# Kernel optimization log

Hardware: AMD Instinct MI355X
Metric: run time of the kernel (lower is better)

## Reference

```python
import jax, jax.numpy as jnp
import numpy as np

B, S, T, D, H, V, R = 16, 100, 60, 512, 8, 32000, 20
DK = D // H
WIN = 20
DECAY1 = (jnp.arange(WIN, dtype=jnp.float32) + 1.0) / 20.0  # decay1[i] = (i+1)/20


def _add_state_init():
    # decay2[:S] padded with zeros: decay2[i] = 1 - (i+1)/50 for i < 50
    idx = jnp.arange(S, dtype=jnp.float32)
    return jnp.where(idx < 50, 1.0 - (idx + 1.0) / 50.0, 0.0)  # [S]


def _forward(v_outputs, f_outputs, query_seq, attn_logits, Wr, br, Wa, ba, Wq_lin,
             Wn, bn, Wlogit, blogit, Wptr, bptr, Wqr, bqr, Wkr, bkr, src_mask):
    dt = v_outputs.dtype
    add0 = _add_state_init().astype(dt)
    mem0 = v_outputs * add0[None, :, None]                       # [B,S,D]
    add_state0 = jnp.broadcast_to(add0[None, :, None], (B, S, 1)).astype(dt)
    # role_selector keys, computed once (queries change per step)
    k_heads = (f_outputs @ Wkr + bkr).reshape(B, R, H, DK).transpose(0, 2, 1, 3)  # [B,H,R,DK]
    abuf0 = jnp.zeros((WIN, B, S), dt)   # last-20 attn weights (oldest first)
    qbuf0 = jnp.zeros((WIN, B, D), dt)   # last-20 decoder states

    def step(carry, xs):
        mem, add_state, abuf, qbuf, t = carry
        logits_t, q_t = xs               # [B,S], [B,D]
        # masked softmax over frames (uniformed_this in original)
        attn_i = jax.nn.softmax(jnp.where(src_mask, logits_t, -jnp.inf), axis=-1)  # [B,S]
        # memory read: selected_frame = bmm(attn, memory_bank)
        sel = jnp.einsum('bs,bsd->bd', attn_i, mem)
        # role_selector multi-head attention weights (mean over heads)
        qh = (sel @ Wqr + bqr).reshape(B, H, DK)
        scores = jnp.einsum('bhk,bhrk->bhr', qh, k_heads) / jnp.sqrt(jnp.asarray(DK, dt))
        role_attn = jax.nn.softmax(scores, axis=-1).mean(axis=1)  # [B,R]
        # pointer-generator joint distribution
        vocab = q_t @ Wlogit.T + blogit                            # [B,V] (tied embedding)
        p_gen = jax.nn.sigmoid(q_t @ Wptr + bptr)                  # [B,1]
        joint = jnp.concatenate([vocab, role_attn * p_gen], axis=-1)  # [B,V+R]
        # slide 20-step window buffers
        abuf = jnp.concatenate([abuf[1:], attn_i[None]], axis=0)
        qbuf = jnp.concatenate([qbuf[1:], q_t[None]], axis=0)
        # decay-weighted sums: temp = softmax(decay1[20-L:]) over valid window
        L = jnp.minimum(t + 1, WIN)
        w = jax.nn.softmax(jnp.where(jnp.arange(WIN) >= WIN - L, DECAY1, -jnp.inf)).astype(dt)
        attn_w = jnp.einsum('k,kbs->bs', w, abuf)                  # [B,S]
        query_w = jnp.einsum('k,kbd->bd', w, qbuf)                 # [B,D]
        # gated remove
        rem = jax.nn.sigmoid(q_t @ Wr + br)[:, :, None]            # [B,1,1]
        addp = jax.nn.sigmoid(q_t @ Wa + ba)[:, :, None]           # [B,1,1]
        sim = jax.nn.sigmoid(jnp.einsum('bsd,bd->bs', mem, query_w @ Wq_lin.T))[:, :, None]
        mem = mem * (1.0 - rem * attn_w[:, :, None] * sim)
        # gated add
        last_ctx = jnp.einsum('bs,bsd->bd', attn_w, v_outputs)[:, None, :]  # [B,1,D]
        nxt = jax.nn.sigmoid(
            jnp.concatenate([v_outputs, jnp.broadcast_to(last_ctx, (B, S, D))], axis=-1) @ Wn + bn)  # [B,S,1]
        gain = addp * nxt
        mem = mem + v_outputs * (1.0 - add_state) * gain
        add_state = add_state + (1.0 - add_state) * gain
        return (mem, add_state, abuf, qbuf, t + 1), joint

    xs = (attn_logits.transpose(1, 0, 2), query_seq.transpose(1, 0, 2))
    _, joints = jax.lax.scan(step, (mem0, add_state0, abuf0, qbuf0, 0), xs)
    return joints.transpose(1, 0, 2)  # [B,T,V+R]


def setup_inputs() -> dict:
    key = jax.random.key(0)
    ks = jax.random.split(key, 12)
    n = jax.random.normal
    sd = 0.02
    return {
        'v_outputs': n(ks[0], (B, S, D), jnp.float32),
        'f_outputs': n(ks[1], (B, R, D), jnp.float32),
        'query_seq': n(ks[2], (B, T, D), jnp.float32),
        'attn_logits': n(ks[3], (B, T, S), jnp.float32),
        'Wr': n(ks[4], (D, 1), jnp.float32) * sd, 'br': jnp.zeros((1,), jnp.float32),
        'Wa': n(ks[5], (D, 1), jnp.float32) * sd, 'ba': jnp.zeros((1,), jnp.float32),
        'Wq_lin': n(ks[6], (D, D), jnp.float32) * sd,
        'Wn': n(ks[7], (2 * D, 1), jnp.float32) * sd, 'bn': jnp.zeros((1,), jnp.float32),
        'Wlogit': n(ks[8], (V, D), jnp.float32) * sd, 'blogit': jnp.zeros((V,), jnp.float32),
        'Wptr': n(ks[9], (D, 1), jnp.float32) * sd, 'bptr': jnp.zeros((1,), jnp.float32),
        'Wqr': n(ks[10], (D, D), jnp.float32) * sd, 'bqr': jnp.zeros((D,), jnp.float32),
        'Wkr': n(ks[11], (D, D), jnp.float32) * sd, 'bkr': jnp.zeros((D,), jnp.float32),
        'src_mask': jnp.ones((B, S), dtype=bool),
    }


def reference(v_outputs, f_outputs, query_seq, attn_logits, Wr, br, Wa, ba, Wq_lin,
              Wn, bn, Wlogit, blogit, Wptr, bptr, Wqr, bqr, Wkr, bkr, src_mask):
    return _forward(v_outputs, f_outputs, query_seq, attn_logits, Wr, br, Wa, ba, Wq_lin,
                    Wn, bn, Wlogit, blogit, Wptr, bptr, Wqr, bqr, Wkr, bkr, src_mask)
```

## Files before the change

kernel.cpp:

```cpp
#include <hip/hip_runtime.h>
#include <math.h>

constexpr int B = 16, S = 100, T = 60, D = 512, H = 8, V = 32000, R = 20;
constexpr int DK = 64, WIN = 20;
constexpr int VR = V + R;
constexpr int BT = B * T;
constexpr int MP = 1024;
constexpr int TP = 64;
constexpr int FP = 384;
constexpr int VBP = 1664;

typedef unsigned short u16;
typedef __attribute__((ext_vector_type(8))) short bf16x8;
typedef __attribute__((ext_vector_type(4))) float f32x4;

__device__ __forceinline__ float wred_sum(float v) {
#pragma unroll
  for (int st = 32; st > 0; st >>= 1) v += __shfl_xor(v, st, 64);
  return v;
}
__device__ __forceinline__ float wred_max(float v) {
#pragma unroll
  for (int st = 32; st > 0; st >>= 1) v = fmaxf(v, __shfl_xor(v, st, 64));
  return v;
}
__device__ __forceinline__ float sigmoidf_(float x) { return 1.f / (1.f + expf(-x)); }
__device__ __forceinline__ u16 f2bf(float x) {
  unsigned u = __float_as_uint(x);
  return (u16)((u + 0x7fffu + ((u >> 16) & 1u)) >> 16);
}
__device__ __forceinline__ void gload_lds16(const u16* g, u16* l) {
  __builtin_amdgcn_global_load_lds((const __attribute__((address_space(1))) void*)g,
                                   (__attribute__((address_space(3))) void*)l, 16, 0, 0);
}


__device__ __forceinline__ void vn_body(int row, int l, const float* __restrict__ v,
                                        const float* __restrict__ Wn,
                                        float* __restrict__ vn, float* __restrict__ vn2) {
  const float* vr = v + (size_t)row * D + l * 8;
  float p0 = 0.f, p1 = 0.f;
#pragma unroll
  for (int i = 0; i < 8; i++) {
    float x = vr[i];
    p0 = fmaf(x, Wn[l * 8 + i], p0);
    p1 = fmaf(x, Wn[D + l * 8 + i], p1);
  }
  p0 = wred_sum(p0); p1 = wred_sum(p1);
  if (l == 0) { vn[row] = p0; vn2[row] = p1; }
}

__device__ __forceinline__ void attnscal_body(int row, int l,
    const float* __restrict__ logits, const float* __restrict__ q,
    const float* __restrict__ Wr, const float* __restrict__ br,
    const float* __restrict__ Wa, const float* __restrict__ ba,
    const float* __restrict__ Wptr, const float* __restrict__ bptr,
    float* __restrict__ attn_g, float* __restrict__ remv,
    float* __restrict__ addp, float* __restrict__ pgen) {
  const float* src = logits + (size_t)row * S;
  float a = src[l];
  float b2 = (l + 64 < S) ? src[l + 64] : -INFINITY;
  float m = wred_max(fmaxf(a, b2));
  float ea = expf(a - m), eb = (l + 64 < S) ? expf(b2 - m) : 0.f;
  float inv = 1.f / wred_sum(ea + eb);
  attn_g[(size_t)row * S + l] = ea * inv;
  if (l + 64 < S) attn_g[(size_t)row * S + l + 64] = eb * inv;

  const float* qr = q + (size_t)row * D + l * 8;
  float pr = 0.f, pa = 0.f, pp = 0.f;
#pragma unroll
  for (int i = 0; i < 8; i++) {
    float x = qr[i];
    pr = fmaf(x, Wr[l * 8 + i], pr);
    pa = fmaf(x, Wa[l * 8 + i], pa);
    pp = fmaf(x, Wptr[l * 8 + i], pp);
  }
#pragma unroll
  for (int st = 32; st > 0; st >>= 1) {
    pr += __shfl_xor(pr, st, 64);
    pa += __shfl_xor(pa, st, 64);
    pp += __shfl_xor(pp, st, 64);
  }
  if (l == 0) {
    remv[row] = sigmoidf_(pr + br[0]);
    addp[row] = sigmoidf_(pa + ba[0]);
    pgen[row] = sigmoidf_(pp + bptr[0]);
  }
}

__device__ __forceinline__ void attnw_body(int row, int tid, float* red,
    const float* __restrict__ attn, const float* __restrict__ vn2,
    const float* __restrict__ remv, float* __restrict__ ra, float* __restrict__ ctxn) {
  int b = row / T, t = row % T;
  int L = min(t + 1, WIN);
  if (tid < 128) {
    float dnm = 0.f;
    for (int j = 0; j < L; j++) dnm += expf((float)(WIN - j) / 20.f);
    float p = 0.f;
    if (tid < S) {
      float aw = 0.f;
      for (int j = 0; j < L; j++)
        aw = fmaf(expf((float)(WIN - j) / 20.f) / dnm, attn[(size_t)(row - j) * S + tid], aw);
      ra[(size_t)row * S + tid] = remv[row] * aw;
      p = aw * vn2[b * S + tid];
    }
    red[tid] = p;
  }
  __syncthreads();
  if (tid < 64) {
    float v2 = red[tid] + red[tid + 64];
    v2 = wred_sum(v2);
    if (tid == 0) ctxn[row] = v2;
  }
}

constexpr int NW = V * D / 4;
constexpr int NQ = MP * D / 4;
constexpr int NWQ = D * D / 4;
constexpr int NF = FP * D / 4;
constexpr int NVB = VBP * D / 4;
constexpr int NB_CVT = (NW + NQ + NWQ + NF + NVB) / 256;
constexpr int NB_QWB = MP;
constexpr int NB_PREP = NB_CVT + NB_QWB + 128;
__device__ __forceinline__ void prep_body(int blk, int tid, float (*tile)[65],
    const float* __restrict__ Wlogit, const float* __restrict__ q,
    const float* __restrict__ Wq, const float* __restrict__ f, const float* __restrict__ v,
    const float* __restrict__ Wqr, const float* __restrict__ Wkr,
    u16* __restrict__ Wlbf, u16* __restrict__ qbf,
    u16* __restrict__ Wqlb, u16* __restrict__ fb, u16* __restrict__ vb,
    u16* __restrict__ qwb, u16* __restrict__ WqrT, u16* __restrict__ WkrT) {
  if (blk < NB_CVT) {
    int idx = blk * 256 + tid;
    if (idx < NW) {
      float4 x = reinterpret_cast<const float4*>(Wlogit)[idx];
      ushort4 o = {f2bf(x.x), f2bf(x.y), f2bf(x.z), f2bf(x.w)};
      reinterpret_cast<ushort4*>(Wlbf)[idx] = o;
    } else if (idx < NW + NQ) {
      int j = idx - NW;
      int row = (j * 4) / D;
      ushort4 o = {0, 0, 0, 0};
      if (row < BT) {
        float4 x = reinterpret_cast<const float4*>(q)[j];
        o = {f2bf(x.x), f2bf(x.y), f2bf(x.z), f2bf(x.w)};
      }
      reinterpret_cast<ushort4*>(qbf)[j] = o;
    } else if (idx < NW + NQ + NWQ) {
      int j = idx - NW - NQ;
      float4 x = reinterpret_cast<const float4*>(Wq)[j];
      ushort4 o = {f2bf(x.x), f2bf(x.y), f2bf(x.z), f2bf(x.w)};
      reinterpret_cast<ushort4*>(Wqlb)[j] = o;
    } else if (idx < NW + NQ + NWQ + NF) {
      int j = idx - NW - NQ - NWQ;
      int row = (j * 4) / D;
      ushort4 o = {0, 0, 0, 0};
      if (row < B * R) {
        float4 x = reinterpret_cast<const float4*>(f)[j];
        o = {f2bf(x.x), f2bf(x.y), f2bf(x.z), f2bf(x.w)};
      }
      reinterpret_cast<ushort4*>(fb)[j] = o;
    } else {
      int j = idx - NW - NQ - NWQ - NF;
      int row = (j * 4) / D;
      ushort4 o = {0, 0, 0, 0};
      if (row < B * S) {
        float4 x = reinterpret_cast<const float4*>(v)[j];
        o = {f2bf(x.x), f2bf(x.y), f2bf(x.z), f2bf(x.w)};
      }
      reinterpret_cast<ushort4*>(vb)[j] = o;
    }
  } else if (blk < NB_CVT + NB_QWB) {
    int row = blk - NB_CVT;
    if (row >= BT) {
      qwb[(size_t)row * D + tid] = 0; qwb[(size_t)row * D + tid + 256] = 0;
      return;
    }
    int t = row % T, L = min(t + 1, WIN);
    float dnm = 0.f;
    for (int j = 0; j < L; j++) dnm += expf((float)(WIN - j) / 20.f);
    float a0 = 0.f, a1 = 0.f;
    for (int j = 0; j < L; j++) {
      float wj = expf((float)(WIN - j) / 20.f) / dnm;
      a0 = fmaf(wj, q[(size_t)(row - j) * D + tid], a0);
      a1 = fmaf(wj, q[(size_t)(row - j) * D + tid + 256], a1);
    }
    qwb[(size_t)row * D + tid] = f2bf(a0);
    qwb[(size_t)row * D + tid + 256] = f2bf(a1);
  } else {
    int qt = blk - NB_CVT - NB_QWB;
    const float* src = (qt < 64) ? Wqr : Wkr;
    u16* dst = (qt < 64) ? WqrT : WkrT;
    int q64 = qt & 63;
    int bx = q64 % 8, by = q64 / 8;
#pragma unroll
    for (int i = 0; i < 16; i++) {
      int e = i * 256 + tid, r = e >> 6, c = e & 63;
      tile[r][c] = src[(size_t)(by * 64 + r) * D + bx * 64 + c];
    }
    __syncthreads();
#pragma unroll
    for (int i = 0; i < 16; i++) {
      int e = i * 256 + tid, r = e >> 6, c = e & 63;
      dst[(size_t)(bx * 64 + r) * D + by * 64 + c] = f2bf(tile[c][r]);
    }
  }
}

__device__ __forceinline__ void gemm512_body(const u16* __restrict__ A, const u16* __restrict__ Bw,
                                             const float* __restrict__ bias, float* __restrict__ outp,
                                             int mlimit, int mt, int nt, int tid, u16* ldsbuf) {
  u16* As = ldsbuf;
  u16* Bs = ldsbuf + 128 * 64;
  int m0 = mt * 128, n0 = nt * 128;
  int l = tid & 63;
  int w = tid >> 6, wm = w >> 1, wn = w & 1;
  f32x4 acc[4][4];
#pragma unroll
  for (int mb = 0; mb < 4; mb++)
#pragma unroll
    for (int nb = 0; nb < 4; nb++) acc[mb][nb] = (f32x4){0.f, 0.f, 0.f, 0.f};

  for (int k0 = 0; k0 < D; k0 += 64) {
#pragma unroll
    for (int i = 0; i < 4; i++) {
      int chunk = i * 256 + tid;
      int row = chunk >> 3, kc = chunk & 7;
      int kcs = kc ^ (row & 7);
      gload_lds16(A + (size_t)(m0 + row) * D + k0 + kcs * 8, As + chunk * 8);
      gload_lds16(Bw + (size_t)(n0 + row) * D + k0 + kcs * 8, Bs + chunk * 8);
    }
    __syncthreads();
#pragma unroll
    for (int kk = 0; kk < 2; kk++) {
      bf16x8 af[4], bfr[4];
#pragma unroll
      for (int mb = 0; mb < 4; mb++) {
        int row = wm * 64 + mb * 16 + (l & 15);
        int kc0 = kk * 4 + (l >> 4);
        af[mb] = *(const bf16x8*)(As + row * 64 + ((kc0 ^ (row & 7)) << 3));
      }
#pragma unroll
      for (int nb = 0; nb < 4; nb++) {
        int row = wn * 64 + nb * 16 + (l & 15);
        int kc0 = kk * 4 + (l >> 4);
        bfr[nb] = *(const bf16x8*)(Bs + row * 64 + ((kc0 ^ (row & 7)) << 3));
      }
#pragma unroll
      for (int mb = 0; mb < 4; mb++)
#pragma unroll
        for (int nb = 0; nb < 4; nb++)
          acc[mb][nb] = __builtin_amdgcn_mfma_f32_16x16x32_bf16(af[mb], bfr[nb], acc[mb][nb], 0, 0, 0);
    }
    __syncthreads();
  }

  float* ch = (float*)ldsbuf;
#pragma unroll
  for (int c = 0; c < 4; c++) {
    if (wm == (c >> 1)) {
#pragma unroll
      for (int nb = 0; nb < 4; nb++) {
        int col = wn * 64 + nb * 16 + (l & 15);
        float bl = bias ? bias[n0 + col] : 0.f;
#pragma unroll
        for (int mbi = 0; mbi < 2; mbi++) {
          int mb = (c & 1) * 2 + mbi;
#pragma unroll
          for (int q2 = 0; q2 < 4; q2++) {
            int row_local = mb * 16 + (l >> 4) * 4 + q2 - (c & 1) * 32;
            ch[row_local * 132 + col] = acc[mb][nb][q2] + bl;
          }
        }
      }
    }
    __syncthreads();
#pragma unroll
    for (int p = 0; p < 4; p++) {
      int r = p * 8 + (tid >> 5);
      int m = m0 + c * 32 + r;
      if (m < mlimit) {
        int seg = tid & 31;
        *(float4*)(outp + (size_t)m * D + n0 + seg * 4) =
            *(const float4*)(ch + r * 132 + seg * 4);
      }
    }
    __syncthreads();
  }
}

__device__ __forceinline__ void vocab_body(int bid, int tid, u16* ldsbuf,
    const u16* __restrict__ A, const u16* __restrict__ Bw,
    const float* __restrict__ blog, float* __restrict__ out) {
  u16* As = ldsbuf;
  u16* Bs = ldsbuf + 128 * 64;
  int swz = (bid & 7) * 250 + (bid >> 3);
  int m0 = (swz & 7) * 128, n0 = (swz >> 3) * 128;
  int l = tid & 63;
  int w = tid >> 6, wm = w >> 1, wn = w & 1;

  f32x4 acc[4][4];
#pragma unroll
  for (int mb = 0; mb < 4; mb++)
#pragma unroll
    for (int nb = 0; nb < 4; nb++) acc[mb][nb] = (f32x4){0.f, 0.f, 0.f, 0.f};

  for (int k0 = 0; k0 < D; k0 += 64) {
#pragma unroll
    for (int i = 0; i < 4; i++) {
      int chunk = i * 256 + tid;
      int row = chunk >> 3, kc = chunk & 7;
      int kcs = kc ^ (row & 7);
      gload_lds16(A + (size_t)(m0 + row) * D + k0 + kcs * 8, As + chunk * 8);
      gload_lds16(Bw + (size_t)(n0 + row) * D + k0 + kcs * 8, Bs + chunk * 8);
    }
    __syncthreads();
#pragma unroll
    for (int kk = 0; kk < 2; kk++) {
      bf16x8 af[4], bfr[4];
#pragma unroll
      for (int mb = 0; mb < 4; mb++) {
        int row = wm * 64 + mb * 16 + (l & 15);
        int kc0 = kk * 4 + (l >> 4);
        af[mb] = *(const bf16x8*)(As + row * 64 + ((kc0 ^ (row & 7)) << 3));
      }
#pragma unroll
      for (int nb = 0; nb < 4; nb++) {
        int row = wn * 64 + nb * 16 + (l & 15);
        int kc0 = kk * 4 + (l >> 4);
        bfr[nb] = *(const bf16x8*)(Bs + row * 64 + ((kc0 ^ (row & 7)) << 3));
      }
#pragma unroll
      for (int mb = 0; mb < 4; mb++)
#pragma unroll
        for (int nb = 0; nb < 4; nb++)
          acc[mb][nb] = __builtin_amdgcn_mfma_f32_16x16x32_bf16(af[mb], bfr[nb], acc[mb][nb], 0, 0, 0);
    }
    __syncthreads();
  }

  float* ch = (float*)ldsbuf;
#pragma unroll
  for (int c = 0; c < 4; c++) {
    if (wm == (c >> 1)) {
#pragma unroll
      for (int nb = 0; nb < 4; nb++) {
        int col = wn * 64 + nb * 16 + (l & 15);
        float bl = blog[n0 + col];
#pragma unroll
        for (int mbi = 0; mbi < 2; mbi++) {
          int mb = (c & 1) * 2 + mbi;
#pragma unroll
          for (int q2 = 0; q2 < 4; q2++) {
            int row_local = mb * 16 + (l >> 4) * 4 + q2 - (c & 1) * 32;
            ch[row_local * 132 + col] = acc[mb][nb][q2] + bl;
          }
        }
      }
    }
    __syncthreads();
#pragma unroll
    for (int p = 0; p < 4; p++) {
      int r = p * 8 + (tid >> 5);
      int m = m0 + c * 32 + r;
      if (m < BT) {
        int seg = tid & 31;
        *(float4*)(out + (size_t)m * VR + n0 + seg * 4) =
            *(const float4*)(ch + r * 132 + seg * 4);
      }
    }
    __syncthreads();
  }
}

__device__ __forceinline__ void qhgemm_body(int bq, int tid, float* gT ,
    const float* __restrict__ vWqr, const float* __restrict__ gammaT,
    const float* __restrict__ bqr, float* __restrict__ qh) {
  int b = bq >> 2, dc = bq & 3;
  int dl = tid & 127, th0 = tid >> 7;
  int d = dc * 128 + dl;
  for (int i = tid; i < S * TP; i += 256) {
    int r = i >> 6, c = i & 63;
    gT[r * TP + c] = gammaT[((size_t)b * S + r) * TP + c];
  }
  __syncthreads();
  float acc[2][16];
#pragma unroll
  for (int g = 0; g < 2; g++)
#pragma unroll
    for (int m = 0; m < 16; m++) acc[g][m] = 0.f;
  for (int ss = 0; ss < S; ss++) {
    float vv = vWqr[((size_t)b * S + ss) * D + d];
#pragma unroll
    for (int g = 0; g < 2; g++) {
      int tg = th0 + 2 * g;
      const float* gp = gT + ss * TP + tg * 16;
      float4 g0 = *(const float4*)gp;
      float4 g1 = *(const float4*)(gp + 4);
      float4 g2 = *(const float4*)(gp + 8);
      float4 g3 = *(const float4*)(gp + 12);
      acc[g][0]  = fmaf(g0.x, vv, acc[g][0]);  acc[g][1]  = fmaf(g0.y, vv, acc[g][1]);
      acc[g][2]  = fmaf(g0.z, vv, acc[g][2]);  acc[g][3]  = fmaf(g0.w, vv, acc[g][3]);
      acc[g][4]  = fmaf(g1.x, vv, acc[g][4]);  acc[g][5]  = fmaf(g1.y, vv, acc[g][5]);
      acc[g][6]  = fmaf(g1.z, vv, acc[g][6]);  acc[g][7]  = fmaf(g1.w, vv, acc[g][7]);
      acc[g][8]  = fmaf(g2.x, vv, acc[g][8]);  acc[g][9]  = fmaf(g2.y, vv, acc[g][9]);
      acc[g][10] = fmaf(g2.z, vv, acc[g][10]); acc[g][11] = fmaf(g2.w, vv, acc[g][11]);
      acc[g][12] = fmaf(g3.x, vv, acc[g][12]); acc[g][13] = fmaf(g3.y, vv, acc[g][13]);
      acc[g][14] = fmaf(g3.z, vv, acc[g][14]); acc[g][15] = fmaf(g3.w, vv, acc[g][15]);
    }
  }
  float bz = bqr[d];
#pragma unroll
  for (int g = 0; g < 2; g++) {
    int tg = th0 + 2 * g;
#pragma unroll
    for (int m = 0; m < 16; m++) {
      int t = tg * 16 + m;
      if (t < T) qh[((size_t)b * T + t) * D + d] = acc[g][m] + bz;
    }
  }
}

__device__ __forceinline__ void vubeta_body(int bq, int tid, float* sm,
    const float* __restrict__ u, const float* __restrict__ v,
    const float* __restrict__ attn, const float* __restrict__ ra,
    const float* __restrict__ addp, const float* __restrict__ ctxn,
    const float* __restrict__ vn, const float* __restrict__ bn,
    float* __restrict__ gammaT) {
  int b = bq / 5, sc = bq % 5;
  int tq = tid >> 2, sg = tid & 3;
  float* u_s = sm;
  float* v_s = sm + 7920;
  float* aw_s = sm + 10560;
  float* ra_s = sm + 11760;
  float* vu_s = sm + 12960;
  float* gm_s = sm + 14160;
  float* ap_s = sm + 15360;
  float* cx_s = sm + 15420;
  float* vns_s = sm + 15480;
#pragma unroll
  for (int ii = 0; ii < 5; ii++) {
    int i = ii * 256 + tid;
    if (i < T * 20) {
      int t = i / 20, sl = i % 20;
      size_t base = ((size_t)b * T + t) * S + sc * 20 + sl;
      aw_s[t * 20 + sl] = attn[base];
      ra_s[t * 20 + sl] = ra[base];
    }
  }
  if (tid < T) { ap_s[tid] = addp[b * T + tid]; cx_s[tid] = ctxn[b * T + tid]; }
  if (tid >= 64 && tid < 84) vns_s[tid - 64] = vn[b * S + sc * 20 + tid - 64];

  float acc[5] = {0, 0, 0, 0, 0};
  for (int kc = 0; kc < 4; kc++) {
#pragma unroll
    for (int ii = 0; ii < 8; ii++) {
      int i = ii * 256 + tid;
      if (i < 60 * 32) {
        int r = i >> 5, c = (i & 31) * 4;
        *(float4*)&u_s[r * 132 + c] =
            *(const float4*)&u[((size_t)b * T + r) * D + kc * 128 + c];
      }
    }
#pragma unroll
    for (int ii = 0; ii < 3; ii++) {
      int i = ii * 256 + tid;
      if (i < 20 * 32) {
        int r = i >> 5, c = (i & 31) * 4;
        *(float4*)&v_s[r * 132 + c] =
            *(const float4*)&v[((size_t)b * S + sc * 20 + r) * D + kc * 128 + c];
      }
    }
    __syncthreads();
    if (tq < 60) {
#pragma unroll
      for (int e0 = 0; e0 < 128; e0 += 4) {
        float4 uu = *(const float4*)&u_s[tq * 132 + e0];
#pragma unroll
        for (int m = 0; m < 5; m++) {
          float4 vv = *(const float4*)&v_s[(sg * 5 + m) * 132 + e0];
          acc[m] = fmaf(uu.x, vv.x, acc[m]);
          acc[m] = fmaf(uu.y, vv.y, acc[m]);
          acc[m] = fmaf(uu.z, vv.z, acc[m]);
          acc[m] = fmaf(uu.w, vv.w, acc[m]);
        }
      }
    }
    __syncthreads();
  }
  if (tq < 60) {
#pragma unroll
    for (int m = 0; m < 5; m++) vu_s[tq * 20 + sg * 5 + m] = acc[m];
  }
  __syncthreads();
  if (tid < 20) {
    int s = sc * 20 + tid;
    float dec = (s < 50) ? 1.f - (float)(s + 1) / 50.f : 0.f;
    float a = dec, beta = dec;
    float vns = vns_s[tid], bnv = bn[0];
    for (int t = 0; t < T; t++) {
      float g = ap_s[t] * sigmoidf_(vns + cx_s[t] + bnv);
      float wv = (1.f - a) * g;
      a += wv;
      gm_s[t * 20 + tid] = aw_s[t * 20 + tid] * beta;
      beta = beta * (1.f - ra_s[t * 20 + tid] * sigmoidf_(beta * vu_s[t * 20 + tid])) + wv;
    }
  }
  __syncthreads();
#pragma unroll
  for (int ii = 0; ii < 5; ii++) {
    int i = ii * 256 + tid;
    if (i < T * 20) {
      int sl = i / 60, t = i % 60;
      gammaT[((size_t)b * S + sc * 20 + sl) * TP + t] = gm_s[t * 20 + sl];
    }
  }
}

__device__ __forceinline__ void role_body(int row, int tid, float* sc, float* pr,
    const float* __restrict__ khf, const float* __restrict__ qh,
    const float* __restrict__ pgen, float* __restrict__ out) {
  int b = row / T;
  if (tid < H * R) {
    int h = tid / R, r = tid % R;
    const float* qp = qh + (size_t)row * D + h * DK;
    const float* kp = khf + (size_t)(b * R + r) * D + h * DK;
    float acc = 0.f;
#pragma unroll
    for (int i = 0; i < DK; i++) acc = fmaf(qp[i], kp[i], acc);
    sc[tid] = acc * 0.125f;
  }
  __syncthreads();
  if (tid < H) {
    float m = -INFINITY;
    for (int r = 0; r < R; r++) m = fmaxf(m, sc[tid * R + r]);
    float ssum = 0.f;
    for (int r = 0; r < R; r++) { float e = expf(sc[tid * R + r] - m); pr[tid * R + r] = e; ssum += e; }
    float inv = 1.f / ssum;
    for (int r = 0; r < R; r++) pr[tid * R + r] *= inv;
  }
  __syncthreads();
  if (tid < R) {
    float acc = 0.f;
#pragma unroll
    for (int h = 0; h < H; h++) acc += pr[h * R + tid];
    out[(size_t)row * VR + V + tid] = acc * (1.f / H) * pgen[row];
  }
}


__global__ __launch_bounds__(256) void k_combo1(
    const float* Wlogit, const float* q, const float* Wq, const float* f,
    const float* Wqr, const float* Wkr, const float* logits, const float* v,
    const float* Wn, const float* Wr, const float* br, const float* Wa, const float* ba,
    const float* Wptr, const float* bptr,
    u16* Wlbf, u16* qbf, u16* Wqlb, u16* fb, u16* vb, u16* qwb, u16* WqrT, u16* WkrT,
    float* vn, float* vn2, float* attn_g, float* remv, float* addp, float* pgen) {
  __shared__ float tile[64][65];
  int blk = blockIdx.x, tid = threadIdx.x;
  if (blk < NB_PREP) {
    prep_body(blk, tid, tile, Wlogit, q, Wq, f, v, Wqr, Wkr,
              Wlbf, qbf, Wqlb, fb, vb, qwb, WqrT, WkrT);
  } else if (blk < NB_PREP + 400) {
    int row = (blk - NB_PREP) * 4 + (tid >> 6);
    vn_body(row, tid & 63, v, Wn, vn, vn2);
  } else {
    int row = (blk - NB_PREP - 400) * 4 + (tid >> 6);
    attnscal_body(row, tid & 63, logits, q, Wr, br, Wa, ba, Wptr, bptr,
                  attn_g, remv, addp, pgen);
  }
}

__global__ __launch_bounds__(256) void k_combo2(
    const u16* qbf, const u16* Wlbf, const float* blog, float* out,
    const u16* qwb, const u16* Wqlb, float* u,
    const u16* fb, const u16* WkrT, const float* bkr, float* khf,
    const u16* vb, const u16* WqrT, float* vWqr,
    const float* attn, const float* vn2, const float* remv, float* ra, float* ctxn) {
  __shared__ u16 lds[2 * 128 * 64];
  int blk = blockIdx.x, tid = threadIdx.x;
  if (blk < 550) {
    vocab_body(blk, tid, lds, qbf, Wlbf, blog, out);
  } else if (blk < 594) {
    int z = blk - 550, xx = z % 11, yy = z / 11;
    if (xx < 8) gemm512_body(qwb, Wqlb, nullptr, u, BT, xx, yy, tid, lds);
    else        gemm512_body(fb, WkrT, bkr, khf, B * R, xx - 8, yy, tid, lds);
  } else if (blk < 646) {
    int z = blk - 594;
    gemm512_body(vb, WqrT, nullptr, vWqr, B * S, z % 13, z / 13, tid, lds);
  } else {
    attnw_body(blk - 646, tid, (float*)lds, attn, vn2, remv, ra, ctxn);
  }
}

__global__ __launch_bounds__(256) void k_vubetap(
    const float* u, const float* v, const float* attn, const float* ra,
    const float* addp, const float* ctxn, const float* vn, const float* bn,
    float* gammaT,
    const u16* qbf, const u16* Wlbf, const float* blog, float* out) {
  __shared__ float smem[15500];
  int blk = blockIdx.x, tid = threadIdx.x;
  if (blk < 80) vubeta_body(blk, tid, smem, u, v, attn, ra, addp, ctxn, vn, bn, gammaT);
  else          vocab_body(550 + blk - 80, tid, (u16*)smem, qbf, Wlbf, blog, out);
}

__global__ __launch_bounds__(256) void k_combo3(
    const u16* qbf, const u16* Wlbf, const float* blog, float* out,
    const float* vWqr, const float* gammaT, const float* bqr, float* qh) {
  __shared__ u16 lds[2 * 128 * 64];
  int blk = blockIdx.x, tid = threadIdx.x;
  if (blk < 700) vocab_body(900 + blk, tid, lds, qbf, Wlbf, blog, out);
  else           qhgemm_body(blk - 700, tid, (float*)lds, vWqr, gammaT, bqr, qh);
}

__global__ __launch_bounds__(256) void k_rolep(
    const float* khf, const float* qh, const float* pgen, float* out,
    const u16* qbf, const u16* Wlbf, const float* blog) {
  __shared__ u16 lds[2 * 128 * 64];
  int blk = blockIdx.x, tid = threadIdx.x;
  if (blk < 400) {
    vocab_body(1600 + blk, tid, lds, qbf, Wlbf, blog, out);
  } else {
    float* sc = (float*)lds;
    float* pr = sc + H * R;
    role_body(blk - 400, tid, sc, pr, khf, qh, pgen, out);
  }
}

extern "C" void kernel_launch(void* const* d_in, const int* in_sizes, int n_in,
                              void* d_out, int out_size, void* d_ws, size_t ws_size,
                              hipStream_t stream) {
  const float* v_out  = (const float*)d_in[0];
  const float* f_out  = (const float*)d_in[1];
  const float* q_seq  = (const float*)d_in[2];
  const float* logits = (const float*)d_in[3];
  const float* Wr     = (const float*)d_in[4];
  const float* br     = (const float*)d_in[5];
  const float* Wa     = (const float*)d_in[6];
  const float* ba     = (const float*)d_in[7];
  const float* Wq_lin = (const float*)d_in[8];
  const float* Wn     = (const float*)d_in[9];
  const float* bn     = (const float*)d_in[10];
  const float* Wlogit = (const float*)d_in[11];
  const float* blogit = (const float*)d_in[12];
  const float* Wptr   = (const float*)d_in[13];
  const float* bptr   = (const float*)d_in[14];
  const float* Wqr    = (const float*)d_in[15];
  const float* bqr    = (const float*)d_in[16];
  const float* Wkr    = (const float*)d_in[17];
  const float* bkr    = (const float*)d_in[18];
  float* out = (float*)d_out;
  float* ws  = (float*)d_ws;

  float* attn   = ws;
  float* ra     = attn   + (size_t)BT * S;
  float* u      = ra     + (size_t)BT * S;
  float* pgen   = u      + (size_t)BT * D;
  float* remv   = pgen   + BT;
  float* addp   = remv   + BT;
  float* ctxn   = addp   + BT;
  float* vn     = ctxn   + BT;
  float* vn2    = vn     + B * S;
  float* khf    = vn2    + B * S;
  float* qh     = khf    + (size_t)B * R * D;
  float* gammaT = qh     + (size_t)BT * D;
  float* vWqr   = gammaT + (size_t)B * S * TP;
  u16*   qwb    = (u16*)(vWqr + (size_t)B * S * D);
  u16*   vb     = qwb  + (size_t)MP * D;
  u16*   fb     = vb   + (size_t)VBP * D;
  u16*   Wqlb   = fb   + (size_t)FP * D;
  u16*   WqrT   = Wqlb + (size_t)D * D;
  u16*   WkrT   = WqrT + (size_t)D * D;
  u16*   qbf    = WkrT + (size_t)D * D;
  u16*   Wlbf   = qbf  + (size_t)MP * D;

  k_combo1<<<NB_PREP + 400 + 240, 256, 0, stream>>>(
      Wlogit, q_seq, Wq_lin, f_out, Wqr, Wkr, logits, v_out,
      Wn, Wr, br, Wa, ba, Wptr, bptr,
      Wlbf, qbf, Wqlb, fb, vb, qwb, WqrT, WkrT,
      vn, vn2, attn, remv, addp, pgen);

  k_combo2<<<550 + 44 + 52 + 960, 256, 0, stream>>>(
      qbf, Wlbf, blogit, out, qwb, Wqlb, u, fb, WkrT, bkr, khf,
      vb, WqrT, vWqr, attn, vn2, remv, ra, ctxn);

  k_vubetap<<<80 + 350, 256, 0, stream>>>(
      u, v_out, attn, ra, addp, ctxn, vn, bn, gammaT, qbf, Wlbf, blogit, out);

  k_combo3<<<700 + B * 4, 256, 0, stream>>>(qbf, Wlbf, blogit, out, vWqr, gammaT, bqr, qh);

  k_rolep<<<400 + BT, 256, 0, stream>>>(khf, qh, pgen, out, qbf, Wlbf, blogit);
}
```

Baseline: 172.2 us.

## Reassociate role-query scores via precomputed key-projected memory and drop qh GEMM

Instead of materialising qh = gamma·(v·Wqr)+bqr per step and dotting with role keys, the scores are reassociated: a new per-(batch, head) block computes M = kh·(vWqr)^T plus kh·bqr once, and each role row then dots gamma over S with M. This removes the qh GEMM and its large intermediate, and cuts the kernel count from five to four by merging the vubeta and M stages and rebalancing the vocab blocks across launches. In exchange the role stage does a length-100 reduction per (head, role) instead of length-64, and gamma is stored in a transposed layout.

```diff
diff --git a/kernel.cpp b/kernel.cpp
--- a/kernel.cpp
+++ b/kernel.cpp
@@ -6,7 +6,6 @@
 constexpr int VR = V + R;
 constexpr int BT = B * T;
 constexpr int MP = 1024;
-constexpr int TP = 64;
 constexpr int FP = 384;
 constexpr int VBP = 1664;
 
@@ -371,51 +370,46 @@
   }
 }
 
-__device__ __forceinline__ void qhgemm_body(int bq, int tid, float* gT ,
-    const float* __restrict__ vWqr, const float* __restrict__ gammaT,
-    const float* __restrict__ bqr, float* __restrict__ qh) {
-  int b = bq >> 2, dc = bq & 3;
-  int dl = tid & 127, th0 = tid >> 7;
-  int d = dc * 128 + dl;
-  for (int i = tid; i < S * TP; i += 256) {
-    int r = i >> 6, c = i & 63;
-    gT[r * TP + c] = gammaT[((size_t)b * S + r) * TP + c];
-  }
+__device__ __forceinline__ void mrole_body(int bh, int tid, float* sm,
+    const float* __restrict__ vWqr, const float* __restrict__ khf,
+    const float* __restrict__ bqr, float* __restrict__ M) {
+  int b = bh >> 3, h = bh & 7;
+  float* kh_s = sm;
+  float* vW_s = sm + 1280;
+  float* bq_s = sm + 7680;
+#pragma unroll
+  for (int ii = 0; ii < 2; ii++) {
+    int i = ii * 256 + tid;
+    if (i < 320) {
+      int r = i >> 4, c4 = (i & 15) * 4;
+      *(float4*)&kh_s[r * 64 + c4] =
+          *(const float4*)&khf[(size_t)(b * R + r) * D + h * 64 + c4];
+    }
+  }
+#pragma unroll
+  for (int ii = 0; ii < 7; ii++) {
+    int i = ii * 256 + tid;
+    if (i < 1600) {
+      int s = i >> 4, c4 = (i & 15) * 4;
+      *(float4*)&vW_s[s * 64 + c4] =
+          *(const float4*)&vWqr[(size_t)(b * S + s) * D + h * 64 + c4];
+    }
+  }
+  if (tid < 64) bq_s[tid] = bqr[h * 64 + tid];
   __syncthreads();
-  float acc[2][16];
-#pragma unroll
-  for (int g = 0; g < 2; g++)
-#pragma unroll
-    for (int m = 0; m < 16; m++) acc[g][m] = 0.f;
-  for (int ss = 0; ss < S; ss++) {
-    float vv = vWqr[((size_t)b * S + ss) * D + d];
-#pragma unroll
-    for (int g = 0; g < 2; g++) {
-      int tg = th0 + 2 * g;
-      const float* gp = gT + ss * TP + tg * 16;
-      float4 g0 = *(const float4*)gp;
-      float4 g1 = *(const float4*)(gp + 4);
-      float4 g2 = *(const float4*)(gp + 8);
-      float4 g3 = *(const float4*)(gp + 12);
-      acc[g][0]  = fmaf(g0.x, vv, acc[g][0]);  acc[g][1]  = fmaf(g0.y, vv, acc[g][1]);
-      acc[g][2]  = fmaf(g0.z, vv, acc[g][2]);  acc[g][3]  = fmaf(g0.w, vv, acc[g][3]);
-      acc[g][4]  = fmaf(g1.x, vv, acc[g][4]);  acc[g][5]  = fmaf(g1.y, vv, acc[g][5]);
-      acc[g][6]  = fmaf(g1.z, vv, acc[g][6]);  acc[g][7]  = fmaf(g1.w, vv, acc[g][7]);
-      acc[g][8]  = fmaf(g2.x, vv, acc[g][8]);  acc[g][9]  = fmaf(g2.y, vv, acc[g][9]);
-      acc[g][10] = fmaf(g2.z, vv, acc[g][10]); acc[g][11] = fmaf(g2.w, vv, acc[g][11]);
-      acc[g][12] = fmaf(g3.x, vv, acc[g][12]); acc[g][13] = fmaf(g3.y, vv, acc[g][13]);
-      acc[g][14] = fmaf(g3.z, vv, acc[g][14]); acc[g][15] = fmaf(g3.w, vv, acc[g][15]);
-    }
-  }
-  float bz = bqr[d];
-#pragma unroll
-  for (int g = 0; g < 2; g++) {
-    int tg = th0 + 2 * g;
-#pragma unroll
-    for (int m = 0; m < 16; m++) {
-      int t = tg * 16 + m;
-      if (t < T) qh[((size_t)b * T + t) * D + d] = acc[g][m] + bz;
-    }
+  for (int p = tid; p < R * 104; p += 256) {
+    int r = p / 104, sc = p % 104;
+    if (sc > 100) continue;
+    const float* kp = kh_s + r * 64;
+    const float* xp = (sc < 100) ? (vW_s + sc * 64) : bq_s;
+    float acc = 0.f;
+#pragma unroll
+    for (int e = 0; e < 64; e += 4) {
+      float4 x = *(const float4*)&xp[e];
+      float4 k = *(const float4*)&kp[e];
+      acc = fmaf(x.x, k.x, fmaf(x.y, k.y, fmaf(x.z, k.z, fmaf(x.w, k.w, acc))));
+    }
+    M[(size_t)(bh * R + r) * 104 + sc] = acc;
   }
 }
 
@@ -424,7 +418,7 @@
     const float* __restrict__ attn, const float* __restrict__ ra,
     const float* __restrict__ addp, const float* __restrict__ ctxn,
     const float* __restrict__ vn, const float* __restrict__ bn,
-    float* __restrict__ gammaT) {
+    float* __restrict__ gammaTt) {
   int b = bq / 5, sc = bq % 5;
   int tq = tid >> 2, sg = tid & 3;
   float* u_s = sm;
@@ -509,23 +503,26 @@
   for (int ii = 0; ii < 5; ii++) {
     int i = ii * 256 + tid;
     if (i < T * 20) {
-      int sl = i / 60, t = i % 60;
-      gammaT[((size_t)b * S + sc * 20 + sl) * TP + t] = gm_s[t * 20 + sl];
-    }
-  }
-}
-
-__device__ __forceinline__ void role_body(int row, int tid, float* sc, float* pr,
-    const float* __restrict__ khf, const float* __restrict__ qh,
+      int t = i / 20, sl = i % 20;
+      gammaTt[((size_t)b * T + t) * S + sc * 20 + sl] = gm_s[t * 20 + sl];
+    }
+  }
+}
+
+__device__ __forceinline__ void role_body(int row, int tid, float* sm,
+    const float* __restrict__ M, const float* __restrict__ gammaTt,
     const float* __restrict__ pgen, float* __restrict__ out) {
   int b = row / T;
+  float* gs = sm;
+  float* sc = sm + 104;
+  float* pr = sm + 264;
+  if (tid < S) gs[tid] = gammaTt[(size_t)row * S + tid];
+  __syncthreads();
   if (tid < H * R) {
     int h = tid / R, r = tid % R;
-    const float* qp = qh + (size_t)row * D + h * DK;
-    const float* kp = khf + (size_t)(b * R + r) * D + h * DK;
-    float acc = 0.f;
-#pragma unroll
-    for (int i = 0; i < DK; i++) acc = fmaf(qp[i], kp[i], acc);
+    const float* mp = M + (size_t)((b * H + h) * R + r) * 104;
+    float acc = mp[100];
+    for (int s = 0; s < S; s++) acc = fmaf(gs[s], mp[s], acc);
     sc[tid] = acc * 0.125f;
   }
   __syncthreads();
@@ -577,52 +574,40 @@
     const float* attn, const float* vn2, const float* remv, float* ra, float* ctxn) {
   __shared__ u16 lds[2 * 128 * 64];
   int blk = blockIdx.x, tid = threadIdx.x;
-  if (blk < 550) {
+  if (blk < 600) {
     vocab_body(blk, tid, lds, qbf, Wlbf, blog, out);
-  } else if (blk < 594) {
-    int z = blk - 550, xx = z % 11, yy = z / 11;
+  } else if (blk < 644) {
+    int z = blk - 600, xx = z % 11, yy = z / 11;
     if (xx < 8) gemm512_body(qwb, Wqlb, nullptr, u, BT, xx, yy, tid, lds);
     else        gemm512_body(fb, WkrT, bkr, khf, B * R, xx - 8, yy, tid, lds);
-  } else if (blk < 646) {
-    int z = blk - 594;
+  } else if (blk < 696) {
+    int z = blk - 644;
     gemm512_body(vb, WqrT, nullptr, vWqr, B * S, z % 13, z / 13, tid, lds);
   } else {
-    attnw_body(blk - 646, tid, (float*)lds, attn, vn2, remv, ra, ctxn);
-  }
-}
-
-__global__ __launch_bounds__(256) void k_vubetap(
+    attnw_body(blk - 696, tid, (float*)lds, attn, vn2, remv, ra, ctxn);
+  }
+}
+
+__global__ __launch_bounds__(256) void k_combo3(
     const float* u, const float* v, const float* attn, const float* ra,
     const float* addp, const float* ctxn, const float* vn, const float* bn,
-    float* gammaT,
+    float* gammaTt,
+    const float* vWqr, const float* khf, const float* bqr, float* M,
     const u16* qbf, const u16* Wlbf, const float* blog, float* out) {
   __shared__ float smem[15500];
   int blk = blockIdx.x, tid = threadIdx.x;
-  if (blk < 80) vubeta_body(blk, tid, smem, u, v, attn, ra, addp, ctxn, vn, bn, gammaT);
-  else          vocab_body(550 + blk - 80, tid, (u16*)smem, qbf, Wlbf, blog, out);
-}
-
-__global__ __launch_bounds__(256) void k_combo3(
-    const u16* qbf, const u16* Wlbf, const float* blog, float* out,
-    const float* vWqr, const float* gammaT, const float* bqr, float* qh) {
-  __shared__ u16 lds[2 * 128 * 64];
-  int blk = blockIdx.x, tid = threadIdx.x;
-  if (blk < 700) vocab_body(900 + blk, tid, lds, qbf, Wlbf, blog, out);
-  else           qhgemm_body(blk - 700, tid, (float*)lds, vWqr, gammaT, bqr, qh);
+  if (blk < 80)       vubeta_body(blk, tid, smem, u, v, attn, ra, addp, ctxn, vn, bn, gammaTt);
+  else if (blk < 208) mrole_body(blk - 80, tid, smem, vWqr, khf, bqr, M);
+  else                vocab_body(600 + blk - 208, tid, (u16*)smem, qbf, Wlbf, blog, out);
 }
 
 __global__ __launch_bounds__(256) void k_rolep(
-    const float* khf, const float* qh, const float* pgen, float* out,
+    const float* M, const float* gammaTt, const float* pgen, float* out,
     const u16* qbf, const u16* Wlbf, const float* blog) {
   __shared__ u16 lds[2 * 128 * 64];
   int blk = blockIdx.x, tid = threadIdx.x;
-  if (blk < 400) {
-    vocab_body(1600 + blk, tid, lds, qbf, Wlbf, blog, out);
-  } else {
-    float* sc = (float*)lds;
-    float* pr = sc + H * R;
-    role_body(blk - 400, tid, sc, pr, khf, qh, pgen, out);
-  }
+  if (blk < 800) vocab_body(1200 + blk, tid, lds, qbf, Wlbf, blog, out);
+  else           role_body(blk - 800, tid, (float*)lds, M, gammaTt, pgen, out);
 }
 
 extern "C" void kernel_launch(void* const* d_in, const int* in_sizes, int n_in,
@@ -660,9 +645,9 @@
   float* vn     = ctxn   + BT;
   float* vn2    = vn     + B * S;
   float* khf    = vn2    + B * S;
-  float* qh     = khf    + (size_t)B * R * D;
-  float* gammaT = qh     + (size_t)BT * D;
-  float* vWqr   = gammaT + (size_t)B * S * TP;
+  float* gammaTt= khf    + (size_t)B * R * D;
+  float* M      = gammaTt+ (size_t)BT * S;
+  float* vWqr   = M      + (size_t)B * H * R * 104;
   u16*   qwb    = (u16*)(vWqr + (size_t)B * S * D);
   u16*   vb     = qwb  + (size_t)MP * D;
   u16*   fb     = vb   + (size_t)VBP * D;
@@ -678,14 +663,13 @@
       Wlbf, qbf, Wqlb, fb, vb, qwb, WqrT, WkrT,
       vn, vn2, attn, remv, addp, pgen);
 
-  k_combo2<<<550 + 44 + 52 + 960, 256, 0, stream>>>(
+  k_combo2<<<600 + 44 + 52 + 960, 256, 0, stream>>>(
       qbf, Wlbf, blogit, out, qwb, Wqlb, u, fb, WkrT, bkr, khf,
       vb, WqrT, vWqr, attn, vn2, remv, ra, ctxn);
 
-  k_vubetap<<<80 + 350, 256, 0, stream>>>(
-      u, v_out, attn, ra, addp, ctxn, vn, bn, gammaT, qbf, Wlbf, blogit, out);
-
-  k_combo3<<<700 + B * 4, 256, 0, stream>>>(qbf, Wlbf, blogit, out, vWqr, gammaT, bqr, qh);
-
-  k_rolep<<<400 + BT, 256, 0, stream>>>(khf, qh, pgen, out, qbf, Wlbf, blogit);
-}
+  k_combo3<<<80 + 128 + 600, 256, 0, stream>>>(
+      u, v_out, attn, ra, addp, ctxn, vn, bn, gammaTt,
+      vWqr, khf, bqr, M, qbf, Wlbf, blogit, out);
+
+  k_rolep<<<800 + BT, 256, 0, stream>>>(M, gammaTt, pgen, out, qbf, Wlbf, blogit);
+}
```

Result: no change. 173.4 us (+0.7%).
